# Kernel optimization log

Measured on AMD Instinct MI355X. Metric: run time of the kernel, lower is better.

## Reference

```python
import jax, jax.numpy as jnp
import numpy as np
from jax.scipy.linalg import solve_triangular
from jax.scipy.special import logsumexp

N, K, D = 131072, 32, 32
LOG_2PI = np.float32(np.log(2.0 * np.pi))


def setup_inputs() -> dict:
    key = jax.random.key(0)
    k1, k2, k3, k4 = jax.random.split(key, 4)
    X = jax.random.normal(k1, (N, D), dtype=jnp.float32)
    means = jax.random.normal(k2, (K, D), dtype=jnp.float32)
    chols = jax.random.normal(k3, (K, D, D), dtype=jnp.float32)
    weights = jax.random.normal(k4, (K,), dtype=jnp.float32) - 1.0  # normal_(-1, 1)
    return {"X": X, "means": means, "chols": chols, "weights": weights, "it": 0}


def _neglog_likelihood(X, means, chols, weights):
    d = X.shape[-1]
    n = X.shape[0]
    eye = jnp.eye(d, dtype=X.dtype)
    # sigmas[k] = chols[k] @ chols[k]^T + I  -> (K, D, D)
    sigmas = jnp.einsum('kij,klj->kil', chols, chols) + eye
    L = jnp.linalg.cholesky(sigmas)                      # (K, D, D)
    # per-cluster Gaussian log-densities for all points, batched
    diff = X[None, :, :] - means[:, None, :]             # (K, N, D)
    y = solve_triangular(L, diff.transpose(0, 2, 1), lower=True)  # (K, D, N)
    maha = jnp.sum(y * y, axis=1)                        # (K, N)
    logdet = 2.0 * jnp.sum(jnp.log(jnp.diagonal(L, axis1=-2, axis2=-1)), axis=-1)  # (K,)
    log_dens = -0.5 * (maha + (logdet + d * LOG_2PI)[:, None])    # (K, N)
    dens = jnp.exp(log_dens)                             # (K, N)
    # sum_{i,j} w_i w_j N_i(x) N_j(x) = (sum_k w_k N_k(x))^2
    numer = jnp.square(weights @ dens)                   # (N,)
    # pairwise normaliser Z_ij = N(mu_i; mu_j, S_i + S_j), all pairs batched
    S_ij = sigmas[:, None] + sigmas[None, :]             # (K, K, D, D)
    L_ij = jnp.linalg.cholesky(S_ij)
    dmu = means[:, None, :] - means[None, :, :]          # (K, K, D)
    y_ij = solve_triangular(L_ij, dmu[..., None], lower=True)[..., 0]  # (K, K, D)
    maha_ij = jnp.sum(y_ij * y_ij, axis=-1)              # (K, K)
    logdet_ij = 2.0 * jnp.sum(jnp.log(jnp.diagonal(L_ij, axis1=-2, axis2=-1)), axis=-1)
    Z_ij = jnp.exp(-0.5 * (maha_ij + logdet_ij + d * LOG_2PI))
    z = jnp.sum((weights[:, None] * weights[None, :]) * Z_ij)
    pdf = numer / z                                      # (N,)
    logp = jnp.log(pdf)                                  # (N,)
    return -(logsumexp(logp, axis=0) / n)


def reference(X, means, chols, weights, it):
    return _neglog_likelihood(X, means, chols, weights)
```

## Files before the change

kernel.cpp:

```cpp
#include <hip/hip_runtime.h>
#include <math.h>

#define NPTS  131072
#define NPTB  512
#define NPRB  256
#define GRIDW NPTB
#define DLOG2PIF 58.8120661f
#define DLOG2PI  58.81206612467475
#define SHIFT 92.0f
#define NEGHALF_LOG2E -0.72134752044f
#define LOG2E 1.44269504089f

typedef __attribute__((ext_vector_type(8)))  short short8;
typedef __attribute__((ext_vector_type(16))) float f32x16;

static __device__ __forceinline__ unsigned bfh(float f) {
  unsigned u = __float_as_uint(f);
  return (u + 0x7FFFu + ((u >> 16) & 1u)) >> 16;
}
static __device__ __forceinline__ float bfhf(float f) {
  return __uint_as_float(bfh(f) << 16);
}

__global__ __launch_bounds__(256) void setup_kernel(
    const float* __restrict__ means, const float* __restrict__ chols,
    const float* __restrict__ wts,
    uint4* __restrict__ Afrag, float* __restrict__ gbuf,
    float* __restrict__ Kc, float* __restrict__ Sg,
    double* __restrict__ zterm, unsigned* __restrict__ ticket)
{
  const int tid = threadIdx.x, wv = tid >> 6, lane = tid & 63;
  const int r = lane & 31, h = lane >> 5;
  __shared__ float SshA[4][1056];
  float* Ssh = SshA[wv];
  if (blockIdx.x < 8) {
    const int k = blockIdx.x*4 + wv;
    if (blockIdx.x == 0 && tid == 0) *ticket = 0u;
    const float* cp = chols + (size_t)k*1024 + r*32;
    float4 fa = *(const float4*)(cp + h*8);
    float4 fb = *(const float4*)(cp + h*8 + 4);
    float4 fc = *(const float4*)(cp + 16 + h*8);
    float4 fd = *(const float4*)(cp + 16 + h*8 + 4);
    float v0[8] = {fa.x,fa.y,fa.z,fa.w,fb.x,fb.y,fb.z,fb.w};
    float v1[8] = {fc.x,fc.y,fc.z,fc.w,fd.x,fd.y,fd.z,fd.w};
    short8 hi0, hi1, lo0, lo1;
    #pragma unroll
    for (int j = 0; j < 8; j++) {
      hi0[j] = (short)bfh(v0[j]);  lo0[j] = (short)bfh(v0[j] - bfhf(v0[j]));
      hi1[j] = (short)bfh(v1[j]);  lo1[j] = (short)bfh(v1[j] - bfhf(v1[j]));
    }
    f32x16 acc = {};
    acc = __builtin_amdgcn_mfma_f32_32x32x16_bf16(hi0, hi0, acc, 0,0,0);
    acc = __builtin_amdgcn_mfma_f32_32x32x16_bf16(hi1, hi1, acc, 0,0,0);
    acc = __builtin_amdgcn_mfma_f32_32x32x16_bf16(hi0, lo0, acc, 0,0,0);
    acc = __builtin_amdgcn_mfma_f32_32x32x16_bf16(hi1, lo1, acc, 0,0,0);
    acc = __builtin_amdgcn_mfma_f32_32x32x16_bf16(lo0, hi0, acc, 0,0,0);
    acc = __builtin_amdgcn_mfma_f32_32x32x16_bf16(lo1, hi1, acc, 0,0,0);
    #pragma unroll
    for (int q = 0; q < 16; q++) {
      int row = (q & 3) + 8*(q >> 2) + 4*h;
      Ssh[row*33 + r] = acc[q] + ((row == r) ? 1.0f : 0.0f);
    }
    float a[32];
    #pragma unroll
    for (int j = 0; j < 32; j++) a[j] = Ssh[r*33 + j];
    float ldsum = 0.0f;
    #pragma unroll
    for (int j = 0; j < 32; j++) {
      float dd = __shfl(a[j], j);
      float inv = rsqrtf(dd);
      float sq = dd * inv;
      ldsum += __logf(sq);
      float l = a[j] * inv;
      #pragma unroll
      for (int e = j+1; e < 32; e++) {
        float le = __shfl(l, e);
        a[e] = (r >= e) ? fmaf(-l, le, a[e]) : a[e];
      }
      a[j] = (r == j) ? sq : ((r > j) ? l : a[j]);
    }
    #pragma unroll
    for (int j = 0; j < 32; j++) Ssh[r*33 + j] = a[j];
    float bv[32];
    #pragma unroll
    for (int d = 0; d < 32; d++) {
      float s0 = (d == r) ? 1.0f : 0.0f, s1 = 0.0f;
      #pragma unroll
      for (int j = 0; j + 1 < d; j += 2) {
        s0 = fmaf(-Ssh[d*33 + j],     bv[j],   s0);
        s1 = fmaf(-Ssh[d*33 + j + 1], bv[j+1], s1);
      }
      if (d & 1) s0 = fmaf(-Ssh[d*33 + (d-1)], bv[d-1], s0);
      bv[d] = __fdividef(s0 + s1, Ssh[d*33 + d]);
    }
    #pragma unroll
    for (int d = 0; d < 32; d++) Ssh[d*33 + r] = bv[d];
    float t0[8], t1[8];
    #pragma unroll
    for (int j = 0; j < 8; j++) {
      t0[j] = Ssh[r*33 + h*8 + j];
      t1[j] = Ssh[r*33 + 16 + h*8 + j];
    }
    uint4 s0 = make_uint4(bfh(t0[0])|(bfh(t0[1])<<16), bfh(t0[2])|(bfh(t0[3])<<16),
                          bfh(t0[4])|(bfh(t0[5])<<16), bfh(t0[6])|(bfh(t0[7])<<16));
    uint4 s1 = make_uint4(bfh(t1[0])|(bfh(t1[1])<<16), bfh(t1[2])|(bfh(t1[3])<<16),
                          bfh(t1[4])|(bfh(t1[5])<<16), bfh(t1[6])|(bfh(t1[7])<<16));
    Afrag[(k*2 + 0)*64 + lane] = s0;
    Afrag[(k*2 + 1)*64 + lane] = s1;
    const float* mk = means + k*32;
    float wr = 0.0f;
    #pragma unroll
    for (int j = 0; j < 32; j++) wr = fmaf(bfhf(Ssh[r*33 + j]), mk[j], wr);
    float c = wr*wr;
    #pragma unroll
    for (int off = 16; off > 0; off >>= 1) c += __shfl_xor(c, off);
    float gd = 0.0f;
    #pragma unroll
    for (int rr = 0; rr < 32; rr++)
      gd = fmaf(bfhf(bv[rr]), __shfl(wr, rr), gd);
    if (h == 0) gbuf[k*32 + r] = 2.0f*gd;
    if (lane == 0) {
      float wk = wts[k];
      float ld2 = 2.0f*ldsum + DLOG2PIF;
      Kc[k] = LOG2E*(SHIFT - 0.5f*ld2 - 0.5f*c) + log2f(fabsf(wk));
      Sg[k] = (wk < 0.0f) ? -1.0f : 1.0f;
    }
  } else {
    const int pid = (blockIdx.x - 8)*4 + wv, pi = pid >> 5, pj = pid & 31;
    const float* cpi = chols + (size_t)pi*1024 + r*32;
    const float* cpj = chols + (size_t)pj*1024 + r*32;
    float4 ia = *(const float4*)(cpi + h*8);
    float4 ib = *(const float4*)(cpi + h*8 + 4);
    float4 ic = *(const float4*)(cpi + 16 + h*8);
    float4 id = *(const float4*)(cpi + 16 + h*8 + 4);
    float4 ja = *(const float4*)(cpj + h*8);
    float4 jb = *(const float4*)(cpj + h*8 + 4);
    float4 jc = *(const float4*)(cpj + 16 + h*8);
    float4 jd = *(const float4*)(cpj + 16 + h*8 + 4);
    float vi0[8] = {ia.x,ia.y,ia.z,ia.w,ib.x,ib.y,ib.z,ib.w};
    float vi1[8] = {ic.x,ic.y,ic.z,ic.w,id.x,id.y,id.z,id.w};
    float vj0[8] = {ja.x,ja.y,ja.z,ja.w,jb.x,jb.y,jb.z,jb.w};
    float vj1[8] = {jc.x,jc.y,jc.z,jc.w,jd.x,jd.y,jd.z,jd.w};
    short8 I0h,I0l,I1h,I1l,J0h,J0l,J1h,J1l;
    #pragma unroll
    for (int j = 0; j < 8; j++) {
      I0h[j]=(short)bfh(vi0[j]); I0l[j]=(short)bfh(vi0[j]-bfhf(vi0[j]));
      I1h[j]=(short)bfh(vi1[j]); I1l[j]=(short)bfh(vi1[j]-bfhf(vi1[j]));
      J0h[j]=(short)bfh(vj0[j]); J0l[j]=(short)bfh(vj0[j]-bfhf(vj0[j]));
      J1h[j]=(short)bfh(vj1[j]); J1l[j]=(short)bfh(vj1[j]-bfhf(vj1[j]));
    }
    f32x16 pacc = {};
    pacc = __builtin_amdgcn_mfma_f32_32x32x16_bf16(I0h, I0h, pacc, 0,0,0);
    pacc = __builtin_amdgcn_mfma_f32_32x32x16_bf16(I1h, I1h, pacc, 0,0,0);
    pacc = __builtin_amdgcn_mfma_f32_32x32x16_bf16(I0h, I0l, pacc, 0,0,0);
    pacc = __builtin_amdgcn_mfma_f32_32x32x16_bf16(I1h, I1l, pacc, 0,0,0);
    pacc = __builtin_amdgcn_mfma_f32_32x32x16_bf16(I0l, I0h, pacc, 0,0,0);
    pacc = __builtin_amdgcn_mfma_f32_32x32x16_bf16(I1l, I1h, pacc, 0,0,0);
    pacc = __builtin_amdgcn_mfma_f32_32x32x16_bf16(J0h, J0h, pacc, 0,0,0);
    pacc = __builtin_amdgcn_mfma_f32_32x32x16_bf16(J1h, J1h, pacc, 0,0,0);
    pacc = __builtin_amdgcn_mfma_f32_32x32x16_bf16(J0h, J0l, pacc, 0,0,0);
    pacc = __builtin_amdgcn_mfma_f32_32x32x16_bf16(J1h, J1l, pacc, 0,0,0);
    pacc = __builtin_amdgcn_mfma_f32_32x32x16_bf16(J0l, J0h, pacc, 0,0,0);
    pacc = __builtin_amdgcn_mfma_f32_32x32x16_bf16(J1l, J1h, pacc, 0,0,0);
    #pragma unroll
    for (int q = 0; q < 16; q++) {
      int row = (q & 3) + 8*(q >> 2) + 4*h;
      Ssh[row*33 + r] = pacc[q] + ((row == r) ? 2.0f : 0.0f);
    }
    float a[32];
    #pragma unroll
    for (int j = 0; j < 32; j++) a[j] = Ssh[r*33 + j];
    #pragma unroll
    for (int j = 0; j < 32; j++) {
      float dd = __shfl(a[j], j);
      float inv = __frsqrt_rn(dd);
      float sq = dd * inv;
      float l = a[j] * inv;
      #pragma unroll
      for (int e = j+1; e < 32; e++) {
        float le = __shfl(l, e);
        a[e] = (r >= e) ? fmaf(-l, le, a[e]) : a[e];
      }
      a[j] = (r == j) ? sq : ((r > j) ? l : a[j]);
    }
    float acc2 = means[pi*32 + r] - means[pj*32 + r];
    float maha = 0.0f, ldsum = 0.0f;
    #pragma unroll
    for (int d = 0; d < 32; d++) {
      float dd = __shfl(a[d], d);
      float yd = __shfl(acc2, d) / dd;
      maha = fmaf(yd, yd, maha);
      ldsum += __logf(dd);
      acc2 = (r > d) ? fmaf(-a[d], yd, acc2) : acc2;
    }
    if (lane == 0) {
      double vd = -0.5 * ((double)maha + 2.0*(double)ldsum + DLOG2PI);
      zterm[pid] = (double)wts[pi] * (double)wts[pj] * exp(vd);
    }
  }
}

__global__ __launch_bounds__(256) void work_kernel(
    const float* __restrict__ X,
    const uint4* __restrict__ Afrag, const float* __restrict__ gbuf,
    const float* __restrict__ Kc, const float* __restrict__ Sg,
    const double* __restrict__ zterm, double* __restrict__ partials,
    unsigned* __restrict__ ticket, float* __restrict__ out)
{
  __shared__ __align__(16) uint4 fsh[4096];
  __shared__ float K2sh[32], sksh[32];
  __shared__ double redd[4], redz[4];
  __shared__ unsigned lastFlag;
  const int tid = threadIdx.x, wv = tid >> 6, lane = tid & 63;
  const int r = lane & 31, h = lane >> 5;
  if (tid < 32) { K2sh[tid] = Kc[tid]; sksh[tid] = Sg[tid]; }
  const int n0 = blockIdx.x*256 + wv*64 + r;
  uint4 st[8];
  #pragma unroll
  for (int i = 0; i < 8; i++) st[i] = Afrag[i*256 + tid];
  short8 xh00, xh01, xh10, xh11;
  {
    const float* xp0 = X + (size_t)n0*32;
    const float* xp1 = X + (size_t)(n0+32)*32;
    float4 fa = *(const float4*)(xp0 + h*8);
    float4 fb = *(const float4*)(xp0 + h*8 + 4);
    float4 fc = *(const float4*)(xp0 + 16 + h*8);
    float4 fd = *(const float4*)(xp0 + 16 + h*8 + 4);
    float4 ga = *(const float4*)(xp1 + h*8);
    float4 gb = *(const float4*)(xp1 + h*8 + 4);
    float4 gc = *(const float4*)(xp1 + 16 + h*8);
    float4 gd = *(const float4*)(xp1 + 16 + h*8 + 4);
    float v00[8] = {fa.x,fa.y,fa.z,fa.w,fb.x,fb.y,fb.z,fb.w};
    float v01[8] = {fc.x,fc.y,fc.z,fc.w,fd.x,fd.y,fd.z,fd.w};
    float v10[8] = {ga.x,ga.y,ga.z,ga.w,gb.x,gb.y,gb.z,gb.w};
    float v11[8] = {gc.x,gc.y,gc.z,gc.w,gd.x,gd.y,gd.z,gd.w};
    #pragma unroll
    for (int j = 0; j < 8; j++) {
      xh00[j] = (short)bfh(v00[j]);  xh01[j] = (short)bfh(v01[j]);
      xh10[j] = (short)bfh(v10[j]);  xh11[j] = (short)bfh(v11[j]);
    }
  }
  #pragma unroll
  for (int i = 0; i < 8; i++) fsh[i*256 + tid] = st[i];
  #pragma unroll
  for (int i = 0; i < 8; i++) st[i] = Afrag[(i+8)*256 + tid];
  f32x16 accg0 = {}, accg1 = {};
  {
    const float* gp = gbuf + r*32 + h*8;
    float4 ga = *(const float4*)(gp);
    float4 gb = *(const float4*)(gp + 4);
    float4 gc = *(const float4*)(gp + 16);
    float4 gd = *(const float4*)(gp + 20);
    float g0[8] = {ga.x,ga.y,ga.z,ga.w,gb.x,gb.y,gb.z,gb.w};
    float g1[8] = {gc.x,gc.y,gc.z,gc.w,gd.x,gd.y,gd.z,gd.w};
    short8 Gh0, Gl0, Gh1, Gl1;
    #pragma unroll
    for (int j = 0; j < 8; j++) {
      Gh0[j] = (short)bfh(g0[j]); Gl0[j] = (short)bfh(g0[j] - bfhf(g0[j]));
      Gh1[j] = (short)bfh(g1[j]); Gl1[j] = (short)bfh(g1[j] - bfhf(g1[j]));
    }
    accg0 = __builtin_amdgcn_mfma_f32_32x32x16_bf16(Gh0, xh00, accg0, 0,0,0);
    accg0 = __builtin_amdgcn_mfma_f32_32x32x16_bf16(Gl0, xh00, accg0, 0,0,0);
    accg0 = __builtin_amdgcn_mfma_f32_32x32x16_bf16(Gh1, xh01, accg0, 0,0,0);
    accg0 = __builtin_amdgcn_mfma_f32_32x32x16_bf16(Gl1, xh01, accg0, 0,0,0);
    accg1 = __builtin_amdgcn_mfma_f32_32x32x16_bf16(Gh0, xh10, accg1, 0,0,0);
    accg1 = __builtin_amdgcn_mfma_f32_32x32x16_bf16(Gl0, xh10, accg1, 0,0,0);
    accg1 = __builtin_amdgcn_mfma_f32_32x32x16_bf16(Gh1, xh11, accg1, 0,0,0);
    accg1 = __builtin_amdgcn_mfma_f32_32x32x16_bf16(Gl1, xh11, accg1, 0,0,0);
  }
  #pragma unroll
  for (int i = 0; i < 8; i++) fsh[(i+8)*256 + tid] = st[i];
  __syncthreads();
  const short8* ab = (const short8*)fsh + lane;
  short8 c0 = ab[0], c1 = ab[64];
  float sF0 = 0.0f, sF1 = 0.0f;
  #pragma unroll
  for (int kk = 0; kk < 32; kk++) {
    short8 n0f, n1f;
    if (kk < 31) { n0f = ab[(kk+1)*128]; n1f = ab[(kk+1)*128 + 64]; }
    const float Kk = K2sh[kk], sk = sksh[kk];
    f32x16 acc0 = {}, acc1 = {};
    acc0 = __builtin_amdgcn_mfma_f32_32x32x16_bf16(c0, xh00, acc0, 0,0,0);
    acc0 = __builtin_amdgcn_mfma_f32_32x32x16_bf16(c1, xh01, acc0, 0,0,0);
    acc1 = __builtin_amdgcn_mfma_f32_32x32x16_bf16(c0, xh10, acc1, 0,0,0);
    acc1 = __builtin_amdgcn_mfma_f32_32x32x16_bf16(c1, xh11, acc1, 0,0,0);
    float m0a=0.f, m0b=0.f, m0c=0.f, m0d=0.f;
    float m1a=0.f, m1b=0.f, m1c=0.f, m1d=0.f;
    #pragma unroll
    for (int q = 0; q < 4; q++) {
      m0a = fmaf(acc0[q],    acc0[q],    m0a);
      m0b = fmaf(acc0[q+4],  acc0[q+4],  m0b);
      m0c = fmaf(acc0[q+8],  acc0[q+8],  m0c);
      m0d = fmaf(acc0[q+12], acc0[q+12], m0d);
      m1a = fmaf(acc1[q],    acc1[q],    m1a);
      m1b = fmaf(acc1[q+4],  acc1[q+4],  m1b);
      m1c = fmaf(acc1[q+8],  acc1[q+8],  m1c);
      m1d = fmaf(acc1[q+12], acc1[q+12], m1d);
    }
    const int qg = (kk & 3) | (((kk >> 3) & 3) << 2);
    const int hneed = (kk >> 2) & 1;
    float m0 = (m0a + m0b) + (m0c + m0d) - ((h == hneed) ? accg0[qg] : 0.0f);
    float m1 = (m1a + m1b) + (m1c + m1d) - ((h == hneed) ? accg1[qg] : 0.0f);
    m0 += __shfl_xor(m0, 32);
    m1 += __shfl_xor(m1, 32);
    sF0 = fmaf(sk, exp2f(fmaf(m0, NEGHALF_LOG2E, Kk)), sF0);
    sF1 = fmaf(sk, exp2f(fmaf(m1, NEGHALF_LOG2E, Kk)), sF1);
    c0 = n0f; c1 = n1f;
  }
  double Tp = (double)sF0*(double)sF0 + (double)sF1*(double)sF1;
  if (lane >= 32) Tp = 0.0;
  #pragma unroll
  for (int off = 32; off > 0; off >>= 1) Tp += __shfl_down(Tp, off);
  if (lane == 0) redd[wv] = Tp;
  __syncthreads();
  if (tid == 0) partials[blockIdx.x] = redd[0] + redd[1] + redd[2] + redd[3];
  __syncthreads();
  if (tid == 0) {
    __threadfence();
    lastFlag = (atomicAdd(ticket, 1u) == GRIDW - 1) ? 1u : 0u;
  }
  __syncthreads();
  if (lastFlag) {
    __threadfence();
    double t = 0.0, z = 0.0;
    for (int p = tid; p < NPTB; p += 256) t += partials[p];
    for (int p = tid; p < 1024; p += 256) z += zterm[p];
    #pragma unroll
    for (int off = 32; off > 0; off >>= 1) {
      t += __shfl_down(t, off);
      z += __shfl_down(z, off);
    }
    if (lane == 0) { redd[wv] = t; redz[wv] = z; }
    __syncthreads();
    if (tid == 0) {
      t = redd[0] + redd[1] + redd[2] + redd[3];
      z = redz[0] + redz[1] + redz[2] + redz[3];
      double logT = log(t) - 2.0*(double)SHIFT;
      double logz = log(z);
      out[0] = (float)((logz - logT) / (double)NPTS);
    }
  }
}

extern "C" void kernel_launch(void* const* d_in, const int* in_sizes, int n_in,
                              void* d_out, int out_size, void* d_ws, size_t ws_size,
                              hipStream_t stream) {
  const float* X     = (const float*)d_in[0];
  const float* means = (const float*)d_in[1];
  const float* chols = (const float*)d_in[2];
  const float* wts   = (const float*)d_in[3];
  float* out = (float*)d_out;
  char* ws = (char*)d_ws;
  uint4*    Afrag    = (uint4*)ws;
  float*    gbuf     = (float*)(ws + 65536);
  float*    Kc       = (float*)(ws + 69632);
  float*    Sg       = (float*)(ws + 69760);
  double*   zterm    = (double*)(ws + 69888);
  double*   partials = (double*)(ws + 78080);
  unsigned* ticket   = (unsigned*)(ws + 82176);

  setup_kernel<<<8 + NPRB, 256, 0, stream>>>(means, chols, wts, Afrag, gbuf,
                                             Kc, Sg, zterm, ticket);
  work_kernel<<<GRIDW, 256, 0, stream>>>(X, Afrag, gbuf, Kc, Sg,
                                         zterm, partials, ticket, out);
}
```

Baseline: 114.1 us.

## Move pairwise normaliser blocks into work kernel and use 512-thread blocks

The 1024 pairwise Z_ij Cholesky computations move out of the setup kernel and into extra blocks of the main work kernel. The setup kernel now only factors the 32 per-cluster covariances. The point-processing blocks grow to 512 threads, 512 points per block, with the whole A-fragment table staged into LDS in one pass. This shortens the serial setup kernel and lets the pairwise work overlap with the per-point work, at the cost of a larger LDS footprint and mixed block types in one grid.

```diff
diff --git a/kernel.cpp b/kernel.cpp
--- a/kernel.cpp
+++ b/kernel.cpp
@@ -2,9 +2,9 @@
 #include <math.h>
 
 #define NPTS  131072
-#define NPTB  512
-#define NPRB  256
-#define GRIDW NPTB
+#define NPTB  256
+#define NPRB  128
+#define GRIDW (NPTB + NPRB)
 #define DLOG2PIF 58.8120661f
 #define DLOG2PI  58.81206612467475
 #define SHIFT 92.0f
@@ -27,106 +27,226 @@
     const float* __restrict__ wts,
     uint4* __restrict__ Afrag, float* __restrict__ gbuf,
     float* __restrict__ Kc, float* __restrict__ Sg,
-    double* __restrict__ zterm, unsigned* __restrict__ ticket)
+    unsigned* __restrict__ ticket)
 {
   const int tid = threadIdx.x, wv = tid >> 6, lane = tid & 63;
   const int r = lane & 31, h = lane >> 5;
   __shared__ float SshA[4][1056];
   float* Ssh = SshA[wv];
-  if (blockIdx.x < 8) {
-    const int k = blockIdx.x*4 + wv;
-    if (blockIdx.x == 0 && tid == 0) *ticket = 0u;
-    const float* cp = chols + (size_t)k*1024 + r*32;
-    float4 fa = *(const float4*)(cp + h*8);
-    float4 fb = *(const float4*)(cp + h*8 + 4);
-    float4 fc = *(const float4*)(cp + 16 + h*8);
-    float4 fd = *(const float4*)(cp + 16 + h*8 + 4);
-    float v0[8] = {fa.x,fa.y,fa.z,fa.w,fb.x,fb.y,fb.z,fb.w};
-    float v1[8] = {fc.x,fc.y,fc.z,fc.w,fd.x,fd.y,fd.z,fd.w};
-    short8 hi0, hi1, lo0, lo1;
-    #pragma unroll
-    for (int j = 0; j < 8; j++) {
-      hi0[j] = (short)bfh(v0[j]);  lo0[j] = (short)bfh(v0[j] - bfhf(v0[j]));
-      hi1[j] = (short)bfh(v1[j]);  lo1[j] = (short)bfh(v1[j] - bfhf(v1[j]));
-    }
-    f32x16 acc = {};
-    acc = __builtin_amdgcn_mfma_f32_32x32x16_bf16(hi0, hi0, acc, 0,0,0);
-    acc = __builtin_amdgcn_mfma_f32_32x32x16_bf16(hi1, hi1, acc, 0,0,0);
-    acc = __builtin_amdgcn_mfma_f32_32x32x16_bf16(hi0, lo0, acc, 0,0,0);
-    acc = __builtin_amdgcn_mfma_f32_32x32x16_bf16(hi1, lo1, acc, 0,0,0);
-    acc = __builtin_amdgcn_mfma_f32_32x32x16_bf16(lo0, hi0, acc, 0,0,0);
-    acc = __builtin_amdgcn_mfma_f32_32x32x16_bf16(lo1, hi1, acc, 0,0,0);
-    #pragma unroll
-    for (int q = 0; q < 16; q++) {
-      int row = (q & 3) + 8*(q >> 2) + 4*h;
-      Ssh[row*33 + r] = acc[q] + ((row == r) ? 1.0f : 0.0f);
-    }
-    float a[32];
-    #pragma unroll
-    for (int j = 0; j < 32; j++) a[j] = Ssh[r*33 + j];
-    float ldsum = 0.0f;
-    #pragma unroll
-    for (int j = 0; j < 32; j++) {
-      float dd = __shfl(a[j], j);
-      float inv = rsqrtf(dd);
-      float sq = dd * inv;
-      ldsum += __logf(sq);
-      float l = a[j] * inv;
-      #pragma unroll
-      for (int e = j+1; e < 32; e++) {
-        float le = __shfl(l, e);
-        a[e] = (r >= e) ? fmaf(-l, le, a[e]) : a[e];
+  const int k = blockIdx.x*4 + wv;
+  if (blockIdx.x == 0 && tid == 0) *ticket = 0u;
+  const float* cp = chols + (size_t)k*1024 + r*32;
+  float4 fa = *(const float4*)(cp + h*8);
+  float4 fb = *(const float4*)(cp + h*8 + 4);
+  float4 fc = *(const float4*)(cp + 16 + h*8);
+  float4 fd = *(const float4*)(cp + 16 + h*8 + 4);
+  float v0[8] = {fa.x,fa.y,fa.z,fa.w,fb.x,fb.y,fb.z,fb.w};
+  float v1[8] = {fc.x,fc.y,fc.z,fc.w,fd.x,fd.y,fd.z,fd.w};
+  short8 hi0, hi1, lo0, lo1;
+  #pragma unroll
+  for (int j = 0; j < 8; j++) {
+    hi0[j] = (short)bfh(v0[j]);  lo0[j] = (short)bfh(v0[j] - bfhf(v0[j]));
+    hi1[j] = (short)bfh(v1[j]);  lo1[j] = (short)bfh(v1[j] - bfhf(v1[j]));
+  }
+  f32x16 acc = {};
+  acc = __builtin_amdgcn_mfma_f32_32x32x16_bf16(hi0, hi0, acc, 0,0,0);
+  acc = __builtin_amdgcn_mfma_f32_32x32x16_bf16(hi1, hi1, acc, 0,0,0);
+  acc = __builtin_amdgcn_mfma_f32_32x32x16_bf16(hi0, lo0, acc, 0,0,0);
+  acc = __builtin_amdgcn_mfma_f32_32x32x16_bf16(hi1, lo1, acc, 0,0,0);
+  acc = __builtin_amdgcn_mfma_f32_32x32x16_bf16(lo0, hi0, acc, 0,0,0);
+  acc = __builtin_amdgcn_mfma_f32_32x32x16_bf16(lo1, hi1, acc, 0,0,0);
+  #pragma unroll
+  for (int q = 0; q < 16; q++) {
+    int row = (q & 3) + 8*(q >> 2) + 4*h;
+    Ssh[row*33 + r] = acc[q] + ((row == r) ? 1.0f : 0.0f);
+  }
+  float a[32];
+  #pragma unroll
+  for (int j = 0; j < 32; j++) a[j] = Ssh[r*33 + j];
+  float ldsum = 0.0f;
+  #pragma unroll
+  for (int j = 0; j < 32; j++) {
+    float dd = __shfl(a[j], j);
+    float inv = rsqrtf(dd);
+    float sq = dd * inv;
+    ldsum += __logf(sq);
+    float l = a[j] * inv;
+    #pragma unroll
+    for (int e = j+1; e < 32; e++) {
+      float le = __shfl(l, e);
+      a[e] = (r >= e) ? fmaf(-l, le, a[e]) : a[e];
+    }
+    a[j] = (r == j) ? sq : ((r > j) ? l : a[j]);
+  }
+  #pragma unroll
+  for (int j = 0; j < 32; j++) Ssh[r*33 + j] = a[j];
+  float bv[32];
+  #pragma unroll
+  for (int d = 0; d < 32; d++) {
+    float s0 = (d == r) ? 1.0f : 0.0f, s1 = 0.0f;
+    #pragma unroll
+    for (int j = 0; j + 1 < d; j += 2) {
+      s0 = fmaf(-Ssh[d*33 + j],     bv[j],   s0);
+      s1 = fmaf(-Ssh[d*33 + j + 1], bv[j+1], s1);
+    }
+    if (d & 1) s0 = fmaf(-Ssh[d*33 + (d-1)], bv[d-1], s0);
+    bv[d] = __fdividef(s0 + s1, Ssh[d*33 + d]);
+  }
+  #pragma unroll
+  for (int d = 0; d < 32; d++) Ssh[d*33 + r] = bv[d];
+  float t0[8], t1[8];
+  #pragma unroll
+  for (int j = 0; j < 8; j++) {
+    t0[j] = Ssh[r*33 + h*8 + j];
+    t1[j] = Ssh[r*33 + 16 + h*8 + j];
+  }
+  uint4 s0 = make_uint4(bfh(t0[0])|(bfh(t0[1])<<16), bfh(t0[2])|(bfh(t0[3])<<16),
+                        bfh(t0[4])|(bfh(t0[5])<<16), bfh(t0[6])|(bfh(t0[7])<<16));
+  uint4 s1 = make_uint4(bfh(t1[0])|(bfh(t1[1])<<16), bfh(t1[2])|(bfh(t1[3])<<16),
+                        bfh(t1[4])|(bfh(t1[5])<<16), bfh(t1[6])|(bfh(t1[7])<<16));
+  Afrag[(k*2 + 0)*64 + lane] = s0;
+  Afrag[(k*2 + 1)*64 + lane] = s1;
+  const float* mk = means + k*32;
+  float wr = 0.0f;
+  #pragma unroll
+  for (int j = 0; j < 32; j++) wr = fmaf(bfhf(Ssh[r*33 + j]), mk[j], wr);
+  float c = wr*wr;
+  #pragma unroll
+  for (int off = 16; off > 0; off >>= 1) c += __shfl_xor(c, off);
+  float gd = 0.0f;
+  #pragma unroll
+  for (int rr = 0; rr < 32; rr++)
+    gd = fmaf(bfhf(bv[rr]), __shfl(wr, rr), gd);
+  if (h == 0) gbuf[k*32 + r] = 2.0f*gd;
+  if (lane == 0) {
+    float wk = wts[k];
+    float ld2 = 2.0f*ldsum + DLOG2PIF;
+    Kc[k] = LOG2E*(SHIFT - 0.5f*ld2 - 0.5f*c) + log2f(fabsf(wk));
+    Sg[k] = (wk < 0.0f) ? -1.0f : 1.0f;
+  }
+}
+
+__global__ __launch_bounds__(512) void work_kernel(
+    const float* __restrict__ X, const float* __restrict__ means,
+    const float* __restrict__ chols, const float* __restrict__ wts,
+    const uint4* __restrict__ Afrag, const float* __restrict__ gbuf,
+    const float* __restrict__ Kc, const float* __restrict__ Sg,
+    double* __restrict__ zterm, double* __restrict__ partials,
+    unsigned* __restrict__ ticket, float* __restrict__ out)
+{
+  __shared__ __align__(16) char smem[65536];
+  __shared__ float K2sh[32], sksh[32];
+  __shared__ double redd[8], redz[8];
+  __shared__ unsigned lastFlag;
+  const int tid = threadIdx.x, wv = tid >> 6, lane = tid & 63;
+  const int r = lane & 31, h = lane >> 5;
+  if (blockIdx.x < NPTB) {
+    uint4* fsh = (uint4*)smem;
+    if (tid < 32) { K2sh[tid] = Kc[tid]; sksh[tid] = Sg[tid]; }
+    const int n0 = blockIdx.x*512 + wv*64 + r;
+    uint4 st[8];
+    #pragma unroll
+    for (int i = 0; i < 8; i++) st[i] = Afrag[i*512 + tid];
+    short8 xh00, xh01, xh10, xh11;
+    {
+      const float* xp0 = X + (size_t)n0*32;
+      const float* xp1 = X + (size_t)(n0+32)*32;
+      float4 fa = *(const float4*)(xp0 + h*8);
+      float4 fb = *(const float4*)(xp0 + h*8 + 4);
+      float4 fc = *(const float4*)(xp0 + 16 + h*8);
+      float4 fd = *(const float4*)(xp0 + 16 + h*8 + 4);
+      float4 ga = *(const float4*)(xp1 + h*8);
+      float4 gb = *(const float4*)(xp1 + h*8 + 4);
+      float4 gc = *(const float4*)(xp1 + 16 + h*8);
+      float4 gd = *(const float4*)(xp1 + 16 + h*8 + 4);
+      float v00[8] = {fa.x,fa.y,fa.z,fa.w,fb.x,fb.y,fb.z,fb.w};
+      float v01[8] = {fc.x,fc.y,fc.z,fc.w,fd.x,fd.y,fd.z,fd.w};
+      float v10[8] = {ga.x,ga.y,ga.z,ga.w,gb.x,gb.y,gb.z,gb.w};
+      float v11[8] = {gc.x,gc.y,gc.z,gc.w,gd.x,gd.y,gd.z,gd.w};
+      #pragma unroll
+      for (int j = 0; j < 8; j++) {
+        xh00[j] = (short)bfh(v00[j]);  xh01[j] = (short)bfh(v01[j]);
+        xh10[j] = (short)bfh(v10[j]);  xh11[j] = (short)bfh(v11[j]);
       }
-      a[j] = (r == j) ? sq : ((r > j) ? l : a[j]);
-    }
-    #pragma unroll
-    for (int j = 0; j < 32; j++) Ssh[r*33 + j] = a[j];
-    float bv[32];
-    #pragma unroll
-    for (int d = 0; d < 32; d++) {
-      float s0 = (d == r) ? 1.0f : 0.0f, s1 = 0.0f;
-      #pragma unroll
-      for (int j = 0; j + 1 < d; j += 2) {
-        s0 = fmaf(-Ssh[d*33 + j],     bv[j],   s0);
-        s1 = fmaf(-Ssh[d*33 + j + 1], bv[j+1], s1);
+    }
+    f32x16 accg0 = {}, accg1 = {};
+    {
+      const float* gp = gbuf + r*32 + h*8;
+      float4 ga = *(const float4*)(gp);
+      float4 gb = *(const float4*)(gp + 4);
+      float4 gc = *(const float4*)(gp + 16);
+      float4 gd = *(const float4*)(gp + 20);
+      float g0[8] = {ga.x,ga.y,ga.z,ga.w,gb.x,gb.y,gb.z,gb.w};
+      float g1[8] = {gc.x,gc.y,gc.z,gc.w,gd.x,gd.y,gd.z,gd.w};
+      short8 Gh0, Gl0, Gh1, Gl1;
+      #pragma unroll
+      for (int j = 0; j < 8; j++) {
+        Gh0[j] = (short)bfh(g0[j]); Gl0[j] = (short)bfh(g0[j] - bfhf(g0[j]));
+        Gh1[j] = (short)bfh(g1[j]); Gl1[j] = (short)bfh(g1[j] - bfhf(g1[j]));
       }
-      if (d & 1) s0 = fmaf(-Ssh[d*33 + (d-1)], bv[d-1], s0);
-      bv[d] = __fdividef(s0 + s1, Ssh[d*33 + d]);
-    }
-    #pragma unroll
-    for (int d = 0; d < 32; d++) Ssh[d*33 + r] = bv[d];
-    float t0[8], t1[8];
-    #pragma unroll
-    for (int j = 0; j < 8; j++) {
-      t0[j] = Ssh[r*33 + h*8 + j];
-      t1[j] = Ssh[r*33 + 16 + h*8 + j];
-    }
-    uint4 s0 = make_uint4(bfh(t0[0])|(bfh(t0[1])<<16), bfh(t0[2])|(bfh(t0[3])<<16),
-                          bfh(t0[4])|(bfh(t0[5])<<16), bfh(t0[6])|(bfh(t0[7])<<16));
-    uint4 s1 = make_uint4(bfh(t1[0])|(bfh(t1[1])<<16), bfh(t1[2])|(bfh(t1[3])<<16),
-                          bfh(t1[4])|(bfh(t1[5])<<16), bfh(t1[6])|(bfh(t1[7])<<16));
-    Afrag[(k*2 + 0)*64 + lane] = s0;
-    Afrag[(k*2 + 1)*64 + lane] = s1;
-    const float* mk = means + k*32;
-    float wr = 0.0f;
-    #pragma unroll
-    for (int j = 0; j < 32; j++) wr = fmaf(bfhf(Ssh[r*33 + j]), mk[j], wr);
-    float c = wr*wr;
-    #pragma unroll
-    for (int off = 16; off > 0; off >>= 1) c += __shfl_xor(c, off);
-    float gd = 0.0f;
-    #pragma unroll
-    for (int rr = 0; rr < 32; rr++)
-      gd = fmaf(bfhf(bv[rr]), __shfl(wr, rr), gd);
-    if (h == 0) gbuf[k*32 + r] = 2.0f*gd;
-    if (lane == 0) {
-      float wk = wts[k];
-      float ld2 = 2.0f*ldsum + DLOG2PIF;
-      Kc[k] = LOG2E*(SHIFT - 0.5f*ld2 - 0.5f*c) + log2f(fabsf(wk));
-      Sg[k] = (wk < 0.0f) ? -1.0f : 1.0f;
+      accg0 = __builtin_amdgcn_mfma_f32_32x32x16_bf16(Gh0, xh00, accg0, 0,0,0);
+      accg0 = __builtin_amdgcn_mfma_f32_32x32x16_bf16(Gl0, xh00, accg0, 0,0,0);
+      accg0 = __builtin_amdgcn_mfma_f32_32x32x16_bf16(Gh1, xh01, accg0, 0,0,0);
+      accg0 = __builtin_amdgcn_mfma_f32_32x32x16_bf16(Gl1, xh01, accg0, 0,0,0);
+      accg1 = __builtin_amdgcn_mfma_f32_32x32x16_bf16(Gh0, xh10, accg1, 0,0,0);
+      accg1 = __builtin_amdgcn_mfma_f32_32x32x16_bf16(Gl0, xh10, accg1, 0,0,0);
+      accg1 = __builtin_amdgcn_mfma_f32_32x32x16_bf16(Gh1, xh11, accg1, 0,0,0);
+      accg1 = __builtin_amdgcn_mfma_f32_32x32x16_bf16(Gl1, xh11, accg1, 0,0,0);
+    }
+    #pragma unroll
+    for (int i = 0; i < 8; i++) fsh[i*512 + tid] = st[i];
+    __syncthreads();
+    const short8* ab = (const short8*)fsh + lane;
+    short8 c0 = ab[0], c1 = ab[64];
+    float sF0 = 0.0f, sF1 = 0.0f;
+    #pragma unroll
+    for (int kk = 0; kk < 32; kk++) {
+      short8 n0f, n1f;
+      if (kk < 31) { n0f = ab[(kk+1)*128]; n1f = ab[(kk+1)*128 + 64]; }
+      const float Kk = K2sh[kk], sk = sksh[kk];
+      f32x16 acc0 = {}, acc1 = {};
+      acc0 = __builtin_amdgcn_mfma_f32_32x32x16_bf16(c0, xh00, acc0, 0,0,0);
+      acc0 = __builtin_amdgcn_mfma_f32_32x32x16_bf16(c1, xh01, acc0, 0,0,0);
+      acc1 = __builtin_amdgcn_mfma_f32_32x32x16_bf16(c0, xh10, acc1, 0,0,0);
+      acc1 = __builtin_amdgcn_mfma_f32_32x32x16_bf16(c1, xh11, acc1, 0,0,0);
+      float m0a=0.f, m0b=0.f, m0c=0.f, m0d=0.f;
+      float m1a=0.f, m1b=0.f, m1c=0.f, m1d=0.f;
+      #pragma unroll
+      for (int q = 0; q < 4; q++) {
+        m0a = fmaf(acc0[q],    acc0[q],    m0a);
+        m0b = fmaf(acc0[q+4],  acc0[q+4],  m0b);
+        m0c = fmaf(acc0[q+8],  acc0[q+8],  m0c);
+        m0d = fmaf(acc0[q+12], acc0[q+12], m0d);
+        m1a = fmaf(acc1[q],    acc1[q],    m1a);
+        m1b = fmaf(acc1[q+4],  acc1[q+4],  m1b);
+        m1c = fmaf(acc1[q+8],  acc1[q+8],  m1c);
+        m1d = fmaf(acc1[q+12], acc1[q+12], m1d);
+      }
+      const int qg = (kk & 3) | (((kk >> 3) & 3) << 2);
+      const int hneed = (kk >> 2) & 1;
+      float m0 = (m0a + m0b) + (m0c + m0d) - ((h == hneed) ? accg0[qg] : 0.0f);
+      float m1 = (m1a + m1b) + (m1c + m1d) - ((h == hneed) ? accg1[qg] : 0.0f);
+      m0 += __shfl_xor(m0, 32);
+      m1 += __shfl_xor(m1, 32);
+      sF0 = fmaf(sk, exp2f(fmaf(m0, NEGHALF_LOG2E, Kk)), sF0);
+      sF1 = fmaf(sk, exp2f(fmaf(m1, NEGHALF_LOG2E, Kk)), sF1);
+      c0 = n0f; c1 = n1f;
+    }
+    double Tp = (double)sF0*(double)sF0 + (double)sF1*(double)sF1;
+    if (lane >= 32) Tp = 0.0;
+    #pragma unroll
+    for (int off = 32; off > 0; off >>= 1) Tp += __shfl_down(Tp, off);
+    if (lane == 0) redd[wv] = Tp;
+    __syncthreads();
+    if (tid == 0) {
+      double s = 0.0;
+      #pragma unroll
+      for (int w = 0; w < 8; w++) s += redd[w];
+      partials[blockIdx.x] = s;
     }
   } else {
-    const int pid = (blockIdx.x - 8)*4 + wv, pi = pid >> 5, pj = pid & 31;
+    float* Ssh = (float*)smem + wv*1056;
+    const int pid = (blockIdx.x - NPTB)*8 + wv, pi = pid >> 5, pj = pid & 31;
     const float* cpi = chols + (size_t)pi*1024 + r*32;
     const float* cpj = chols + (size_t)pj*1024 + r*32;
     float4 ia = *(const float4*)(cpi + h*8);
@@ -197,123 +317,8 @@
       double vd = -0.5 * ((double)maha + 2.0*(double)ldsum + DLOG2PI);
       zterm[pid] = (double)wts[pi] * (double)wts[pj] * exp(vd);
     }
-  }
-}
-
-__global__ __launch_bounds__(256) void work_kernel(
-    const float* __restrict__ X,
-    const uint4* __restrict__ Afrag, const float* __restrict__ gbuf,
-    const float* __restrict__ Kc, const float* __restrict__ Sg,
-    const double* __restrict__ zterm, double* __restrict__ partials,
-    unsigned* __restrict__ ticket, float* __restrict__ out)
-{
-  __shared__ __align__(16) uint4 fsh[4096];
-  __shared__ float K2sh[32], sksh[32];
-  __shared__ double redd[4], redz[4];
-  __shared__ unsigned lastFlag;
-  const int tid = threadIdx.x, wv = tid >> 6, lane = tid & 63;
-  const int r = lane & 31, h = lane >> 5;
-  if (tid < 32) { K2sh[tid] = Kc[tid]; sksh[tid] = Sg[tid]; }
-  const int n0 = blockIdx.x*256 + wv*64 + r;
-  uint4 st[8];
-  #pragma unroll
-  for (int i = 0; i < 8; i++) st[i] = Afrag[i*256 + tid];
-  short8 xh00, xh01, xh10, xh11;
-  {
-    const float* xp0 = X + (size_t)n0*32;
-    const float* xp1 = X + (size_t)(n0+32)*32;
-    float4 fa = *(const float4*)(xp0 + h*8);
-    float4 fb = *(const float4*)(xp0 + h*8 + 4);
-    float4 fc = *(const float4*)(xp0 + 16 + h*8);
-    float4 fd = *(const float4*)(xp0 + 16 + h*8 + 4);
-    float4 ga = *(const float4*)(xp1 + h*8);
-    float4 gb = *(const float4*)(xp1 + h*8 + 4);
-    float4 gc = *(const float4*)(xp1 + 16 + h*8);
-    float4 gd = *(const float4*)(xp1 + 16 + h*8 + 4);
-    float v00[8] = {fa.x,fa.y,fa.z,fa.w,fb.x,fb.y,fb.z,fb.w};
-    float v01[8] = {fc.x,fc.y,fc.z,fc.w,fd.x,fd.y,fd.z,fd.w};
-    float v10[8] = {ga.x,ga.y,ga.z,ga.w,gb.x,gb.y,gb.z,gb.w};
-    float v11[8] = {gc.x,gc.y,gc.z,gc.w,gd.x,gd.y,gd.z,gd.w};
-    #pragma unroll
-    for (int j = 0; j < 8; j++) {
-      xh00[j] = (short)bfh(v00[j]);  xh01[j] = (short)bfh(v01[j]);
-      xh10[j] = (short)bfh(v10[j]);  xh11[j] = (short)bfh(v11[j]);
-    }
-  }
-  #pragma unroll
-  for (int i = 0; i < 8; i++) fsh[i*256 + tid] = st[i];
-  #pragma unroll
-  for (int i = 0; i < 8; i++) st[i] = Afrag[(i+8)*256 + tid];
-  f32x16 accg0 = {}, accg1 = {};
-  {
-    const float* gp = gbuf + r*32 + h*8;
-    float4 ga = *(const float4*)(gp);
-    float4 gb = *(const float4*)(gp + 4);
-    float4 gc = *(const float4*)(gp + 16);
-    float4 gd = *(const float4*)(gp + 20);
-    float g0[8] = {ga.x,ga.y,ga.z,ga.w,gb.x,gb.y,gb.z,gb.w};
-    float g1[8] = {gc.x,gc.y,gc.z,gc.w,gd.x,gd.y,gd.z,gd.w};
-    short8 Gh0, Gl0, Gh1, Gl1;
-    #pragma unroll
-    for (int j = 0; j < 8; j++) {
-      Gh0[j] = (short)bfh(g0[j]); Gl0[j] = (short)bfh(g0[j] - bfhf(g0[j]));
-      Gh1[j] = (short)bfh(g1[j]); Gl1[j] = (short)bfh(g1[j] - bfhf(g1[j]));
-    }
-    accg0 = __builtin_amdgcn_mfma_f32_32x32x16_bf16(Gh0, xh00, accg0, 0,0,0);
-    accg0 = __builtin_amdgcn_mfma_f32_32x32x16_bf16(Gl0, xh00, accg0, 0,0,0);
-    accg0 = __builtin_amdgcn_mfma_f32_32x32x16_bf16(Gh1, xh01, accg0, 0,0,0);
-    accg0 = __builtin_amdgcn_mfma_f32_32x32x16_bf16(Gl1, xh01, accg0, 0,0,0);
-    accg1 = __builtin_amdgcn_mfma_f32_32x32x16_bf16(Gh0, xh10, accg1, 0,0,0);
-    accg1 = __builtin_amdgcn_mfma_f32_32x32x16_bf16(Gl0, xh10, accg1, 0,0,0);
-    accg1 = __builtin_amdgcn_mfma_f32_32x32x16_bf16(Gh1, xh11, accg1, 0,0,0);
-    accg1 = __builtin_amdgcn_mfma_f32_32x32x16_bf16(Gl1, xh11, accg1, 0,0,0);
-  }
-  #pragma unroll
-  for (int i = 0; i < 8; i++) fsh[(i+8)*256 + tid] = st[i];
-  __syncthreads();
-  const short8* ab = (const short8*)fsh + lane;
-  short8 c0 = ab[0], c1 = ab[64];
-  float sF0 = 0.0f, sF1 = 0.0f;
-  #pragma unroll
-  for (int kk = 0; kk < 32; kk++) {
-    short8 n0f, n1f;
-    if (kk < 31) { n0f = ab[(kk+1)*128]; n1f = ab[(kk+1)*128 + 64]; }
-    const float Kk = K2sh[kk], sk = sksh[kk];
-    f32x16 acc0 = {}, acc1 = {};
-    acc0 = __builtin_amdgcn_mfma_f32_32x32x16_bf16(c0, xh00, acc0, 0,0,0);
-    acc0 = __builtin_amdgcn_mfma_f32_32x32x16_bf16(c1, xh01, acc0, 0,0,0);
-    acc1 = __builtin_amdgcn_mfma_f32_32x32x16_bf16(c0, xh10, acc1, 0,0,0);
-    acc1 = __builtin_amdgcn_mfma_f32_32x32x16_bf16(c1, xh11, acc1, 0,0,0);
-    float m0a=0.f, m0b=0.f, m0c=0.f, m0d=0.f;
-    float m1a=0.f, m1b=0.f, m1c=0.f, m1d=0.f;
-    #pragma unroll
-    for (int q = 0; q < 4; q++) {
-      m0a = fmaf(acc0[q],    acc0[q],    m0a);
-      m0b = fmaf(acc0[q+4],  acc0[q+4],  m0b);
-      m0c = fmaf(acc0[q+8],  acc0[q+8],  m0c);
-      m0d = fmaf(acc0[q+12], acc0[q+12], m0d);
-      m1a = fmaf(acc1[q],    acc1[q],    m1a);
-      m1b = fmaf(acc1[q+4],  acc1[q+4],  m1b);
-      m1c = fmaf(acc1[q+8],  acc1[q+8],  m1c);
-      m1d = fmaf(acc1[q+12], acc1[q+12], m1d);
-    }
-    const int qg = (kk & 3) | (((kk >> 3) & 3) << 2);
-    const int hneed = (kk >> 2) & 1;
-    float m0 = (m0a + m0b) + (m0c + m0d) - ((h == hneed) ? accg0[qg] : 0.0f);
-    float m1 = (m1a + m1b) + (m1c + m1d) - ((h == hneed) ? accg1[qg] : 0.0f);
-    m0 += __shfl_xor(m0, 32);
-    m1 += __shfl_xor(m1, 32);
-    sF0 = fmaf(sk, exp2f(fmaf(m0, NEGHALF_LOG2E, Kk)), sF0);
-    sF1 = fmaf(sk, exp2f(fmaf(m1, NEGHALF_LOG2E, Kk)), sF1);
-    c0 = n0f; c1 = n1f;
-  }
-  double Tp = (double)sF0*(double)sF0 + (double)sF1*(double)sF1;
-  if (lane >= 32) Tp = 0.0;
-  #pragma unroll
-  for (int off = 32; off > 0; off >>= 1) Tp += __shfl_down(Tp, off);
-  if (lane == 0) redd[wv] = Tp;
-  __syncthreads();
-  if (tid == 0) partials[blockIdx.x] = redd[0] + redd[1] + redd[2] + redd[3];
+    __syncthreads();
+  }
   __syncthreads();
   if (tid == 0) {
     __threadfence();
@@ -323,8 +328,8 @@
   if (lastFlag) {
     __threadfence();
     double t = 0.0, z = 0.0;
-    for (int p = tid; p < NPTB; p += 256) t += partials[p];
-    for (int p = tid; p < 1024; p += 256) z += zterm[p];
+    for (int p = tid; p < NPTB; p += 512) t += partials[p];
+    for (int p = tid; p < 1024; p += 512) z += zterm[p];
     #pragma unroll
     for (int off = 32; off > 0; off >>= 1) {
       t += __shfl_down(t, off);
@@ -333,8 +338,9 @@
     if (lane == 0) { redd[wv] = t; redz[wv] = z; }
     __syncthreads();
     if (tid == 0) {
-      t = redd[0] + redd[1] + redd[2] + redd[3];
-      z = redz[0] + redz[1] + redz[2] + redz[3];
+      t = 0.0; z = 0.0;
+      #pragma unroll
+      for (int w = 0; w < 8; w++) { t += redd[w]; z += redz[w]; }
       double logT = log(t) - 2.0*(double)SHIFT;
       double logz = log(z);
       out[0] = (float)((logz - logT) / (double)NPTS);
@@ -357,10 +363,9 @@
   float*    Sg       = (float*)(ws + 69760);
   double*   zterm    = (double*)(ws + 69888);
   double*   partials = (double*)(ws + 78080);
-  unsigned* ticket   = (unsigned*)(ws + 82176);
-
-  setup_kernel<<<8 + NPRB, 256, 0, stream>>>(means, chols, wts, Afrag, gbuf,
-                                             Kc, Sg, zterm, ticket);
-  work_kernel<<<GRIDW, 256, 0, stream>>>(X, Afrag, gbuf, Kc, Sg,
+  unsigned* ticket   = (unsigned*)(ws + 80128);
+
+  setup_kernel<<<8, 256, 0, stream>>>(means, chols, wts, Afrag, gbuf, Kc, Sg, ticket);
+  work_kernel<<<GRIDW, 512, 0, stream>>>(X, means, chols, wts, Afrag, gbuf, Kc, Sg,
                                          zterm, partials, ticket, out);
 }
```

New measurement: 119.0 us. +4.2%, slower.
